# Kernel tuning notes

Measured on AMD Instinct MI355X. Metric: run time of the kernel, lower is better.

## Reference

```python
import jax, jax.numpy as jnp
import numpy as np
import math

B, N, DIM = 2, 4096, 1024
H, D, M = 16, 64, 256


def setup_inputs() -> dict:
    key = jax.random.key(0)
    ks = jax.random.split(key, 6)
    s = 1.0 / math.sqrt(DIM)
    return {
        "x": jax.random.normal(ks[0], (B, N, DIM), dtype=jnp.float32),
        "w_q": jax.random.normal(ks[1], (DIM, H * D), dtype=jnp.float32) * s,
        "w_k": jax.random.normal(ks[2], (DIM, H * D), dtype=jnp.float32) * s,
        "w_v": jax.random.normal(ks[3], (DIM, H * D), dtype=jnp.float32) * s,
        "w_o": jax.random.normal(ks[4], (H * D, DIM), dtype=jnp.float32) * s,
        "b_o": jnp.zeros((DIM,), dtype=jnp.float32),
        "omega": jax.random.normal(ks[5], (M, D), dtype=jnp.float32),
    }


def _heads(t):
    # [B, N, H*D] -> [B, H, N, D]
    return t.reshape(B, N, H, D).transpose(0, 2, 1, 3)


def _phi(t, omega):
    # t: [B,H,N,D], omega: [M,D] -> [B,H,N,M]
    proj = jnp.einsum("bhnd,md->bhnm", t, omega)
    norm = 0.5 * jnp.sum(t * t, axis=-1, keepdims=True)
    return jnp.exp(proj - norm) / math.sqrt(M)


def reference(x, w_q, w_k, w_v, w_o, b_o, omega):
    q = _heads(x @ w_q)
    k = _heads(x @ w_k)
    v = _heads(x @ w_v)
    phi_q = _phi(q, omega)          # [B,H,N,M]
    phi_k = _phi(k, omega)          # [B,H,N,M]
    kv = jnp.einsum("bhnm,bhnd->bhmd", phi_k, v)   # [B,H,M,D]
    k_sum = phi_k.sum(axis=2)                       # [B,H,M]
    z = 1.0 / (jnp.einsum("bhnm,bhm->bhn", phi_q, k_sum) + 1e-6)
    out = jnp.einsum("bhnm,bhmd->bhnd", phi_q, kv) * z[..., None]
    out = out.transpose(0, 2, 1, 3).reshape(B, N, H * D)
    return out @ w_o + b_o
```

## Files before the change

kernel.cpp:

```cpp
#include <hip/hip_runtime.h>

#define DEVI __device__ __forceinline__

using f32x4 = __attribute__((ext_vector_type(4))) float;
using fvec4 = __attribute__((ext_vector_type(4))) float;
using s16x4 = __attribute__((ext_vector_type(4))) short;
using s16x8 = __attribute__((ext_vector_type(8))) short;

DEVI unsigned short f2bf_rn(float f) {
  union { float f; unsigned u; } v; v.f = f;
  unsigned r = v.u + 0x7fffu + ((v.u >> 16) & 1u);
  return (unsigned short)(r >> 16);
}
DEVI float bf2f(unsigned short h) {
  union { unsigned u; float f; } v; v.u = ((unsigned)h) << 16;
  return v.f;
}
DEVI f32x4 mfma16(s16x8 a, s16x8 b, f32x4 c) {
  return __builtin_amdgcn_mfma_f32_16x16x32_bf16(a, b, c, 0, 0, 0);
}

__global__ __launch_bounds__(256) void k_split_x(
    const float* __restrict__ X,
    unsigned short* __restrict__ XH, unsigned short* __restrict__ XL)
{
  size_t i = ((size_t)blockIdx.x * 256 + threadIdx.x) * 8;
  fvec4 a = *(const fvec4*)&X[i];
  fvec4 b = *(const fvec4*)&X[i + 4];
  s16x8 hv, lv;
#pragma unroll
  for (int j = 0; j < 4; ++j) {
    unsigned short h = f2bf_rn(a[j]);
    hv[j] = (short)h; lv[j] = (short)f2bf_rn(a[j] - bf2f(h));
  }
#pragma unroll
  for (int j = 0; j < 4; ++j) {
    unsigned short h = f2bf_rn(b[j]);
    hv[4 + j] = (short)h; lv[4 + j] = (short)f2bf_rn(b[j] - bf2f(h));
  }
  *(s16x8*)&XH[i] = hv;
  *(s16x8*)&XL[i] = lv;
}

__global__ __launch_bounds__(256) void k_prep_w(
    const float* __restrict__ wq, const float* __restrict__ wk,
    const float* __restrict__ wv, const float* __restrict__ wo,
    unsigned short* __restrict__ WTh, unsigned short* __restrict__ WOT)
{
  __shared__ float tile[64][65];
  const int z = blockIdx.z;
  const float* src = (z == 0) ? wq : (z == 1) ? wk : (z == 2) ? wv : wo;
  const int k0 = blockIdx.x * 64;
  const int n0 = blockIdx.y * 64;
  const int t = threadIdx.x;
#pragma unroll
  for (int j = 0; j < 4; ++j) {
    int r = (t >> 4) + 16 * j;
    int c = (t & 15) * 4;
    fvec4 v = *(const fvec4*)&src[(size_t)(k0 + r) * 1024 + n0 + c];
#pragma unroll
    for (int i = 0; i < 4; ++i) tile[r][c + i] = v[i];
  }
  __syncthreads();
#pragma unroll
  for (int j = 0; j < 4; ++j) {
    int n = (t >> 4) + 16 * j;
    int kc = (t & 15) * 4;
    s16x4 hv;
#pragma unroll
    for (int i = 0; i < 4; ++i) hv[i] = (short)f2bf_rn(tile[kc + i][n]);
    if (z < 3) {
      *(s16x4*)&WTh[(size_t)(z * 1024 + n0 + n) * 1024 + k0 + kc] = hv;
    } else {
      *(s16x4*)&WOT[(size_t)(n0 + n) * 1024 + k0 + kc] = hv;
    }
  }
}

__global__ __launch_bounds__(256) void k_gemm_qkv(
    const unsigned short* __restrict__ XH, const unsigned short* __restrict__ XL,
    const unsigned short* __restrict__ WTh,
    unsigned short* __restrict__ QH, unsigned short* __restrict__ QL,
    unsigned short* __restrict__ KH, unsigned short* __restrict__ KL,
    unsigned short* __restrict__ VB)
{
  __shared__ unsigned short AH[128][40], AL[128][40], BH[128][40];
  const int cb = blockIdx.x;
  const int rb = blockIdx.y;
  const int t = threadIdx.x;
  const int w = t >> 6, l = t & 63;
  const bool tp = (cb < 16);
  f32x4 acc[4][4];
#pragma unroll
  for (int a = 0; a < 4; ++a)
#pragma unroll
    for (int b = 0; b < 4; ++b) acc[a][b] = (f32x4)0.f;

  for (int ks = 0; ks < 32; ++ks) {
    const int k0 = ks * 32;
    {
      int r = t >> 1, c = (t & 1) * 16;
      size_t o = (size_t)(rb * 128 + r) * 1024 + k0 + c;
      *(s16x8*)&AH[r][c]     = *(const s16x8*)&XH[o];
      *(s16x8*)&AH[r][c + 8] = *(const s16x8*)&XH[o + 8];
      if (tp) {
        *(s16x8*)&AL[r][c]     = *(const s16x8*)&XL[o];
        *(s16x8*)&AL[r][c + 8] = *(const s16x8*)&XL[o + 8];
      }
      size_t ob = (size_t)(cb * 128 + r) * 1024 + k0 + c;
      *(s16x8*)&BH[r][c]     = *(const s16x8*)&WTh[ob];
      *(s16x8*)&BH[r][c + 8] = *(const s16x8*)&WTh[ob + 8];
    }
    __syncthreads();
    const int wm = (w & 1) * 64, wn = (w >> 1) * 64;
    const int lr = l & 15, ko = (l >> 4) * 8;
    s16x8 ah[4], al[4], bh[4];
#pragma unroll
    for (int f = 0; f < 4; ++f) {
      ah[f] = *(const s16x8*)&AH[wm + f * 16 + lr][ko];
      bh[f] = *(const s16x8*)&BH[wn + f * 16 + lr][ko];
    }
    if (tp) {
#pragma unroll
      for (int f = 0; f < 4; ++f) al[f] = *(const s16x8*)&AL[wm + f * 16 + lr][ko];
    }
#pragma unroll
    for (int fa = 0; fa < 4; ++fa)
#pragma unroll
      for (int fb = 0; fb < 4; ++fb) {
        acc[fa][fb] = mfma16(ah[fa], bh[fb], acc[fa][fb]);
        if (tp) acc[fa][fb] = mfma16(al[fa], bh[fb], acc[fa][fb]);
      }
    __syncthreads();
  }
  const int wm = (w & 1) * 64, wn = (w >> 1) * 64;
  const int lr = l & 15, lg = l >> 4;
#pragma unroll
  for (int fa = 0; fa < 4; ++fa)
#pragma unroll
    for (int r = 0; r < 4; ++r) {
      int row = rb * 128 + wm + fa * 16 + lg * 4 + r;
#pragma unroll
      for (int fb = 0; fb < 4; ++fb) {
        int col = cb * 128 + wn + fb * 16 + lr;
        float v = acc[fa][fb][r];
        unsigned short hs = f2bf_rn(v);
        if (cb < 8) {
          QH[(size_t)row * 1024 + col] = hs;
          QL[(size_t)row * 1024 + col] = f2bf_rn(v - bf2f(hs));
        } else if (cb < 16) {
          KH[(size_t)row * 1024 + col - 1024] = hs;
          KL[(size_t)row * 1024 + col - 1024] = f2bf_rn(v - bf2f(hs));
        } else {
          VB[(size_t)row * 1024 + col - 2048] = hs;
        }
      }
    }
}

__global__ __launch_bounds__(512, 1) void k_phik_kv(
    const unsigned short* __restrict__ KH, const unsigned short* __restrict__ KL,
    const unsigned short* __restrict__ VB,
    const float* __restrict__ omega, float* __restrict__ KVP)
{
  __shared__ unsigned short OH[256][72];
  __shared__ unsigned short KHs[64][72], KLs[64][72];
  __shared__ unsigned short PKT[256][72];
  __shared__ unsigned short AVT[80][72];
  __shared__ float norm_s[64];
  const int nc = blockIdx.x;
  const int bh = blockIdx.y;
  const int b = bh >> 4, h = bh & 15;
  const int t = threadIdx.x, w = t >> 6, l = t & 63;
  const int lr = l & 15, lg = l >> 4, ko8 = lg * 8;

#pragma unroll
  for (int j = 0; j < 8; ++j) {
    int e = j * 512 + t;
    int m = e >> 4, c = (e & 15) * 4;
    fvec4 v = *(const fvec4*)&omega[m * 64 + c];
    s16x4 hv;
#pragma unroll
    for (int i = 0; i < 4; ++i) hv[i] = (short)f2bf_rn(v[i]);
    *(s16x4*)&OH[m][c] = hv;
  }
  for (int e = t; e < 16 * 64; e += 512) {
    int rr = e >> 6, cc = e & 63;
    AVT[64 + rr][cc] = (rr == 0) ? (unsigned short)0x3F80 : (unsigned short)0;
  }

  f32x4 acc2[5][2];
#pragma unroll
  for (int a = 0; a < 5; ++a)
#pragma unroll
    for (int bb = 0; bb < 2; ++bb) acc2[a][bb] = (f32x4)0.f;

  for (int st = 0; st < 8; ++st) {
    const int n0 = nc * 512 + st * 64;
    __syncthreads();
    {
      int r = t >> 3, c8 = (t & 7) * 8;
      size_t o = (size_t)(b * 4096 + n0 + r) * 1024 + h * 64 + c8;
      s16x8 vh = *(const s16x8*)&KH[o];
      s16x8 vl = *(const s16x8*)&KL[o];
      *(s16x8*)&KHs[r][c8] = vh;
      *(s16x8*)&KLs[r][c8] = vl;
      float ss = 0.f;
#pragma unroll
      for (int i = 0; i < 8; ++i) {
        float q = bf2f((unsigned short)vh[i]) + bf2f((unsigned short)vl[i]);
        ss += q * q;
      }
      ss += __shfl_xor(ss, 1);
      ss += __shfl_xor(ss, 2);
      ss += __shfl_xor(ss, 4);
      if ((t & 7) == 0) norm_s[r] = 0.5f * ss;
    }
    {
      int n = t >> 3, dq = (t & 7) * 8;
      s16x8 v = *(const s16x8*)&VB[(size_t)(b * 4096 + n0 + n) * 1024 + h * 64 + dq];
#pragma unroll
      for (int i = 0; i < 8; ++i) AVT[dq + i][n] = (unsigned short)v[i];
    }
    __syncthreads();
    f32x4 acc[4][2];
#pragma unroll
    for (int a = 0; a < 4; ++a)
#pragma unroll
      for (int bb = 0; bb < 2; ++bb) acc[a][bb] = (f32x4)0.f;
#pragma unroll
    for (int ksub = 0; ksub < 2; ++ksub) {
      int ko = ksub * 32 + ko8;
      s16x8 ah[4], al[4], bh[2];
#pragma unroll
      for (int f = 0; f < 4; ++f) {
        ah[f] = *(const s16x8*)&KHs[f * 16 + lr][ko];
        al[f] = *(const s16x8*)&KLs[f * 16 + lr][ko];
      }
#pragma unroll
      for (int f = 0; f < 2; ++f) bh[f] = *(const s16x8*)&OH[w * 32 + f * 16 + lr][ko];
#pragma unroll
      for (int fa = 0; fa < 4; ++fa)
#pragma unroll
        for (int fb = 0; fb < 2; ++fb) {
          acc[fa][fb] = mfma16(ah[fa], bh[fb], acc[fa][fb]);
          acc[fa][fb] = mfma16(al[fa], bh[fb], acc[fa][fb]);
        }
    }
#pragma unroll
    for (int fa = 0; fa < 4; ++fa)
#pragma unroll
      for (int r = 0; r < 4; ++r) {
        int n = fa * 16 + lg * 4 + r;
        float nm = norm_s[n];
#pragma unroll
        for (int fb = 0; fb < 2; ++fb) {
          int m = w * 32 + fb * 16 + lr;
          float p = __expf(acc[fa][fb][r] - nm) * 0.0625f;
          PKT[m][n] = f2bf_rn(p);
        }
      }
    __syncthreads();
#pragma unroll
    for (int ksub = 0; ksub < 2; ++ksub) {
      int ko = ksub * 32 + ko8;
      s16x8 fA[5], fB[2];
#pragma unroll
      for (int f = 0; f < 5; ++f) fA[f] = *(const s16x8*)&AVT[f * 16 + lr][ko];
#pragma unroll
      for (int f = 0; f < 2; ++f) fB[f] = *(const s16x8*)&PKT[w * 32 + f * 16 + lr][ko];
#pragma unroll
      for (int fa = 0; fa < 5; ++fa)
#pragma unroll
        for (int fb = 0; fb < 2; ++fb) acc2[fa][fb] = mfma16(fA[fa], fB[fb], acc2[fa][fb]);
    }
  }
#pragma unroll
  for (int fa = 0; fa < 5; ++fa)
#pragma unroll
    for (int r = 0; r < 4; ++r) {
      int dp = fa * 16 + lg * 4 + r;
#pragma unroll
      for (int fb = 0; fb < 2; ++fb) {
        int m = w * 32 + fb * 16 + lr;
        KVP[(size_t)((bh * 8 + nc) * 80 + dp) * 256 + m] = acc2[fa][fb][r];
      }
    }
}

__global__ __launch_bounds__(256) void k_kv_reduce(
    const float* __restrict__ KVP, float* __restrict__ KVT)
{
  int idx = blockIdx.x * 256 + threadIdx.x;
  if (idx >= 32 * 80 * 256) return;
  int bh = idx / (80 * 256);
  int rem = idx % (80 * 256);
  float s = 0.f;
#pragma unroll
  for (int nci = 0; nci < 8; ++nci) s += KVP[(size_t)(bh * 8 + nci) * 80 * 256 + rem];
  KVT[idx] = s;
}

__global__ __launch_bounds__(256) void k_phi_q(
    const unsigned short* __restrict__ QH, const unsigned short* __restrict__ QL,
    const float* __restrict__ omega,
    unsigned short* __restrict__ PHIQ)
{
  __shared__ unsigned short AHs[64][72], ALs[64][72];
  __shared__ unsigned short OH[256][72];
  __shared__ float norm_s[64];
  const int nt = blockIdx.x;
  const int bh = blockIdx.y;
  const int t = threadIdx.x, w = t >> 6, l = t & 63;
  const int b = bh >> 4, h = bh & 15;
  {
    int r = t >> 2, cq = (t & 3) * 4;
    float ss = 0.f;
#pragma unroll
    for (int j = 0; j < 4; ++j) {
      int c = cq + 16 * j;
      size_t o = (size_t)(b * 4096 + nt * 64 + r) * 1024 + h * 64 + c;
      s16x4 vh = *(const s16x4*)&QH[o];
      s16x4 vl = *(const s16x4*)&QL[o];
      *(s16x4*)&AHs[r][c] = vh;
      *(s16x4*)&ALs[r][c] = vl;
#pragma unroll
      for (int i = 0; i < 4; ++i) {
        float q = bf2f((unsigned short)vh[i]) + bf2f((unsigned short)vl[i]);
        ss += q * q;
      }
    }
    ss += __shfl_xor(ss, 1);
    ss += __shfl_xor(ss, 2);
    if ((t & 3) == 0) norm_s[r] = 0.5f * ss;
  }
#pragma unroll
  for (int j = 0; j < 16; ++j) {
    int e = j * 256 + t;
    int m = e >> 4, c = (e & 15) * 4;
    fvec4 v = *(const fvec4*)&omega[m * 64 + c];
    s16x4 hv;
#pragma unroll
    for (int i = 0; i < 4; ++i) hv[i] = (short)f2bf_rn(v[i]);
    *(s16x4*)&OH[m][c] = hv;
  }
  __syncthreads();
  f32x4 acc[4][4];
#pragma unroll
  for (int a = 0; a < 4; ++a)
#pragma unroll
    for (int bb = 0; bb < 4; ++bb) acc[a][bb] = (f32x4)0.f;
  const int lr = l & 15, ko8 = (l >> 4) * 8;
#pragma unroll
  for (int ksub = 0; ksub < 2; ++ksub) {
    int ko = ksub * 32 + ko8;
    s16x8 ah[4], al[4], bh[4];
#pragma unroll
    for (int f = 0; f < 4; ++f) {
      ah[f] = *(const s16x8*)&AHs[f * 16 + lr][ko];
      al[f] = *(const s16x8*)&ALs[f * 16 + lr][ko];
      bh[f] = *(const s16x8*)&OH[w * 64 + f * 16 + lr][ko];
    }
#pragma unroll
    for (int fa = 0; fa < 4; ++fa)
#pragma unroll
      for (int fb = 0; fb < 4; ++fb) {
        acc[fa][fb] = mfma16(ah[fa], bh[fb], acc[fa][fb]);
        acc[fa][fb] = mfma16(al[fa], bh[fb], acc[fa][fb]);
      }
  }
  const int lg = l >> 4;
#pragma unroll
  for (int fa = 0; fa < 4; ++fa)
#pragma unroll
    for (int r = 0; r < 4; ++r) {
      int n = fa * 16 + lg * 4 + r;
      float nm = norm_s[n];
#pragma unroll
      for (int fb = 0; fb < 4; ++fb) {
        int m = w * 64 + fb * 16 + lr;
        float p = __expf(acc[fa][fb][r] - nm) * 0.0625f;
        PHIQ[(size_t)(bh * 4096 + nt * 64 + n) * 256 + m] = f2bf_rn(p);
      }
    }
}

__global__ __launch_bounds__(256) void k_attn(
    const unsigned short* __restrict__ PHIQ,
    const float* __restrict__ KVT,
    unsigned short* __restrict__ ATT)
{
  __shared__ unsigned short KVB[80][264];
  __shared__ unsigned short PH[128][40];
  const int ntile = blockIdx.x;
  const int bh = blockIdx.y;
  const int b = bh >> 4, h = bh & 15;
  const int t = threadIdx.x, w = t >> 6, l = t & 63;
#pragma unroll
  for (int j = 0; j < 20; ++j) {
    int e = (j * 256 + t) * 4;
    int dp = e >> 8, m = e & 255;
    fvec4 v = *(const fvec4*)&KVT[(size_t)bh * 80 * 256 + dp * 256 + m];
    s16x4 hv;
#pragma unroll
    for (int i = 0; i < 4; ++i) hv[i] = (short)f2bf_rn(v[i]);
    *(s16x4*)&KVB[dp][m] = hv;
  }
  __syncthreads();
  f32x4 acc[2][5];
#pragma unroll
  for (int a = 0; a < 2; ++a)
#pragma unroll
    for (int bb = 0; bb < 5; ++bb) acc[a][bb] = (f32x4)0.f;
  for (int ks = 0; ks < 8; ++ks) {
    const int m0 = ks * 32;
#pragma unroll
    for (int j = 0; j < 2; ++j) {
      int n = t >> 1, c = (t & 1) * 8 + j * 16;
      *(s16x8*)&PH[n][c] =
          *(const s16x8*)&PHIQ[(size_t)(bh * 4096 + ntile * 128 + n) * 256 + m0 + c];
    }
    __syncthreads();
    const int lr = l & 15, ko = (l >> 4) * 8;
    s16x8 fA[2], fB[5];
#pragma unroll
    for (int f = 0; f < 2; ++f) fA[f] = *(const s16x8*)&PH[w * 32 + f * 16 + lr][ko];
#pragma unroll
    for (int f = 0; f < 5; ++f) fB[f] = *(const s16x8*)&KVB[f * 16 + lr][m0 + ko];
#pragma unroll
    for (int fa = 0; fa < 2; ++fa)
#pragma unroll
      for (int fb = 0; fb < 5; ++fb) acc[fa][fb] = mfma16(fA[fa], fB[fb], acc[fa][fb]);
    __syncthreads();
  }
  const int lr = l & 15, lg = l >> 4;
#pragma unroll
  for (int fa = 0; fa < 2; ++fa)
#pragma unroll
    for (int r = 0; r < 4; ++r) {
      float den = __shfl(acc[fa][4][r], (l & 48));
      float z = 1.f / (den + 1e-6f);
      int n = ntile * 128 + w * 32 + fa * 16 + lg * 4 + r;
#pragma unroll
      for (int fb = 0; fb < 4; ++fb) {
        int col = h * 64 + fb * 16 + lr;
        ATT[(size_t)(b * 4096 + n) * 1024 + col] = f2bf_rn(acc[fa][fb][r] * z);
      }
    }
}

__global__ __launch_bounds__(256) void k_gemm_out(
    const unsigned short* __restrict__ ATT,
    const unsigned short* __restrict__ WOT,
    const float* __restrict__ b_o,
    float* __restrict__ OUT)
{
  __shared__ unsigned short As[128][40], Bs[128][40];
  const int cb = blockIdx.x;
  const int rb = blockIdx.y;
  const int t = threadIdx.x, w = t >> 6, l = t & 63;
  f32x4 acc[4][4];
#pragma unroll
  for (int a = 0; a < 4; ++a)
#pragma unroll
    for (int bb = 0; bb < 4; ++bb) acc[a][bb] = (f32x4)0.f;
  for (int ks = 0; ks < 32; ++ks) {
    const int k0 = ks * 32;
#pragma unroll
    for (int j = 0; j < 2; ++j) {
      int r = t >> 1, c = (t & 1) * 8 + j * 16;
      *(s16x8*)&As[r][c] = *(const s16x8*)&ATT[(size_t)(rb * 128 + r) * 1024 + k0 + c];
      *(s16x8*)&Bs[r][c] = *(const s16x8*)&WOT[(size_t)(cb * 128 + r) * 1024 + k0 + c];
    }
    __syncthreads();
    const int wm = (w & 1) * 64, wn = (w >> 1) * 64, lr = l & 15, ko = (l >> 4) * 8;
    s16x8 fA[4], fB[4];
#pragma unroll
    for (int f = 0; f < 4; ++f) {
      fA[f] = *(const s16x8*)&As[wm + f * 16 + lr][ko];
      fB[f] = *(const s16x8*)&Bs[wn + f * 16 + lr][ko];
    }
#pragma unroll
    for (int fa = 0; fa < 4; ++fa)
#pragma unroll
      for (int fb = 0; fb < 4; ++fb) acc[fa][fb] = mfma16(fA[fa], fB[fb], acc[fa][fb]);
    __syncthreads();
  }
  const int wm = (w & 1) * 64, wn = (w >> 1) * 64, lr = l & 15, lg = l >> 4;
#pragma unroll
  for (int fa = 0; fa < 4; ++fa)
#pragma unroll
    for (int r = 0; r < 4; ++r) {
      int row = rb * 128 + wm + fa * 16 + lg * 4 + r;
#pragma unroll
      for (int fb = 0; fb < 4; ++fb) {
        int col = cb * 128 + wn + fb * 16 + lr;
        OUT[(size_t)row * 1024 + col] = acc[fa][fb][r] + b_o[col];
      }
    }
}

extern "C" void kernel_launch(void* const* d_in, const int* in_sizes, int n_in,
                              void* d_out, int out_size, void* d_ws, size_t ws_size,
                              hipStream_t stream)
{
  const float* x  = (const float*)d_in[0];
  const float* wq = (const float*)d_in[1];
  const float* wk = (const float*)d_in[2];
  const float* wv = (const float*)d_in[3];
  const float* wo = (const float*)d_in[4];
  const float* bo = (const float*)d_in[5];
  const float* om = (const float*)d_in[6];
  float* out = (float*)d_out;

  const size_t PLANE = (size_t)8192 * 1024 * 2;
  char* ws = (char*)d_ws;
  unsigned short* WOT = (unsigned short*)(ws);
  char* segB = ws + 2097152;
  char* segC = segB + 2 * PLANE;
  char* segD = segC + 4 * PLANE;
  char* segE = segD + 26214400;

  unsigned short* QH  = (unsigned short*)segB;
  unsigned short* QL  = (unsigned short*)(segB + PLANE);
  unsigned short* ATT = (unsigned short*)segB;

  unsigned short* KH  = (unsigned short*)segC;
  unsigned short* KL  = (unsigned short*)(segC + PLANE);
  unsigned short* VB  = (unsigned short*)(segC + 2 * PLANE);
  unsigned short* XH  = (unsigned short*)(segC + 3 * PLANE);
  unsigned short* PHIQ = (unsigned short*)segC;

  unsigned short* WTh = (unsigned short*)segD;
  unsigned short* XL  = (unsigned short*)(segD + 6291456);
  float* KVP = (float*)segD;
  float* KVT = (float*)segE;

  k_split_x<<<dim3(4096), 256, 0, stream>>>(x, XH, XL);
  k_prep_w<<<dim3(16, 16, 4), 256, 0, stream>>>(wq, wk, wv, wo, WTh, WOT);
  k_gemm_qkv<<<dim3(24, 64), 256, 0, stream>>>(XH, XL, WTh, QH, QL, KH, KL, VB);
  k_phik_kv<<<dim3(8, 32), 512, 0, stream>>>(KH, KL, VB, om, KVP);
  k_kv_reduce<<<dim3(2560), 256, 0, stream>>>(KVP, KVT);
  k_phi_q<<<dim3(64, 32), 256, 0, stream>>>(QH, QL, om, PHIQ);
  k_attn<<<dim3(32, 32), 256, 0, stream>>>(PHIQ, KVT, ATT);
  k_gemm_out<<<dim3(8, 64), 256, 0, stream>>>(ATT, WOT, bo, out);
}
```

Baseline: 256.3 us.

## Fuse phi_q with attention and use direct global-to-LDS loads in GEMMs

Merges the phi(Q) feature-map kernel and the attention kernel, so phi_q stays in shared memory instead of going through a global buffer. QKV and output GEMMs now stage tiles with global_load_lds 16-byte loads into unpadded LDS. This removes the PHIQ global round trip and register staging. In exchange, the fused kernel uses a large LDS footprint, which limits occupancy, and the unpadded layout may cause bank conflicts.

```diff
diff --git a/kernel.cpp b/kernel.cpp
--- a/kernel.cpp
+++ b/kernel.cpp
@@ -18,6 +18,11 @@
 }
 DEVI f32x4 mfma16(s16x8 a, s16x8 b, f32x4 c) {
   return __builtin_amdgcn_mfma_f32_16x16x32_bf16(a, b, c, 0, 0, 0);
+}
+DEVI void gld16(const void* g, void* lds) {
+  __builtin_amdgcn_global_load_lds(
+      (const __attribute__((address_space(1))) unsigned int*)g,
+      (__attribute__((address_space(3))) unsigned int*)lds, 16, 0, 0);
 }
 
 __global__ __launch_bounds__(256) void k_split_x(
@@ -84,7 +89,7 @@
     unsigned short* __restrict__ KH, unsigned short* __restrict__ KL,
     unsigned short* __restrict__ VB)
 {
-  __shared__ unsigned short AH[128][40], AL[128][40], BH[128][40];
+  __shared__ unsigned short AH[128 * 32], AL[128 * 32], BH[128 * 32];
   const int cb = blockIdx.x;
   const int rb = blockIdx.y;
   const int t = threadIdx.x;
@@ -96,33 +101,43 @@
 #pragma unroll
     for (int b = 0; b < 4; ++b) acc[a][b] = (f32x4)0.f;
 
+  const int r0 = w * 32;
+  const int lrow = l >> 2;
+  const int lcol = (l & 3) * 8;
+  const size_t gA0 = (size_t)(rb * 128 + r0 + lrow) * 1024 + lcol;
+  const size_t gA1 = gA0 + (size_t)16 * 1024;
+  const size_t gB0 = (size_t)(cb * 128 + r0 + lrow) * 1024 + lcol;
+  const size_t gB1 = gB0 + (size_t)16 * 1024;
+  unsigned short* ldsA0 = &AH[r0 * 32];
+  unsigned short* ldsA1 = &AH[(r0 + 16) * 32];
+  unsigned short* ldsL0 = &AL[r0 * 32];
+  unsigned short* ldsL1 = &AL[(r0 + 16) * 32];
+  unsigned short* ldsB0 = &BH[r0 * 32];
+  unsigned short* ldsB1 = &BH[(r0 + 16) * 32];
+
+  const int wm = (w & 1) * 64, wn = (w >> 1) * 64;
+  const int lr = l & 15, ko = (l >> 4) * 8;
+
   for (int ks = 0; ks < 32; ++ks) {
     const int k0 = ks * 32;
-    {
-      int r = t >> 1, c = (t & 1) * 16;
-      size_t o = (size_t)(rb * 128 + r) * 1024 + k0 + c;
-      *(s16x8*)&AH[r][c]     = *(const s16x8*)&XH[o];
-      *(s16x8*)&AH[r][c + 8] = *(const s16x8*)&XH[o + 8];
-      if (tp) {
-        *(s16x8*)&AL[r][c]     = *(const s16x8*)&XL[o];
-        *(s16x8*)&AL[r][c + 8] = *(const s16x8*)&XL[o + 8];
-      }
-      size_t ob = (size_t)(cb * 128 + r) * 1024 + k0 + c;
-      *(s16x8*)&BH[r][c]     = *(const s16x8*)&WTh[ob];
-      *(s16x8*)&BH[r][c + 8] = *(const s16x8*)&WTh[ob + 8];
-    }
-    __syncthreads();
-    const int wm = (w & 1) * 64, wn = (w >> 1) * 64;
-    const int lr = l & 15, ko = (l >> 4) * 8;
+    gld16(&XH[gA0 + k0], ldsA0);
+    gld16(&XH[gA1 + k0], ldsA1);
+    if (tp) {
+      gld16(&XL[gA0 + k0], ldsL0);
+      gld16(&XL[gA1 + k0], ldsL1);
+    }
+    gld16(&WTh[gB0 + k0], ldsB0);
+    gld16(&WTh[gB1 + k0], ldsB1);
+    __syncthreads();
     s16x8 ah[4], al[4], bh[4];
 #pragma unroll
     for (int f = 0; f < 4; ++f) {
-      ah[f] = *(const s16x8*)&AH[wm + f * 16 + lr][ko];
-      bh[f] = *(const s16x8*)&BH[wn + f * 16 + lr][ko];
+      ah[f] = *(const s16x8*)&AH[(wm + f * 16 + lr) * 32 + ko];
+      bh[f] = *(const s16x8*)&BH[(wn + f * 16 + lr) * 32 + ko];
     }
     if (tp) {
 #pragma unroll
-      for (int f = 0; f < 4; ++f) al[f] = *(const s16x8*)&AL[wm + f * 16 + lr][ko];
+      for (int f = 0; f < 4; ++f) al[f] = *(const s16x8*)&AL[(wm + f * 16 + lr) * 32 + ko];
     }
 #pragma unroll
     for (int fa = 0; fa < 4; ++fa)
@@ -133,8 +148,7 @@
       }
     __syncthreads();
   }
-  const int wm = (w & 1) * 64, wn = (w >> 1) * 64;
-  const int lr = l & 15, lg = l >> 4;
+  const int lg = l >> 4;
 #pragma unroll
   for (int fa = 0; fa < 4; ++fa)
 #pragma unroll
@@ -301,18 +315,22 @@
   KVT[idx] = s;
 }
 
-__global__ __launch_bounds__(256) void k_phi_q(
-    const unsigned short* __restrict__ QH, const unsigned short* __restrict__ QL,
-    const float* __restrict__ omega,
-    unsigned short* __restrict__ PHIQ)
-{
-  __shared__ unsigned short AHs[64][72], ALs[64][72];
+__global__ __launch_bounds__(256) void k_phiq_attn(
+    const unsigned short* QH, const unsigned short* QL,
+    const float* __restrict__ omega, const float* __restrict__ KVT,
+    unsigned short* ATT)
+{
+  __shared__ unsigned short QHs[64][72], QLs[64][72];
   __shared__ unsigned short OH[256][72];
+  __shared__ unsigned short PQ[64][264];
+  __shared__ unsigned short KVB[80][264];
   __shared__ float norm_s[64];
   const int nt = blockIdx.x;
   const int bh = blockIdx.y;
   const int t = threadIdx.x, w = t >> 6, l = t & 63;
   const int b = bh >> 4, h = bh & 15;
+  const int lr = l & 15, lg = l >> 4, ko8 = lg * 8;
+
   {
     int r = t >> 2, cq = (t & 3) * 4;
     float ss = 0.f;
@@ -322,8 +340,8 @@
       size_t o = (size_t)(b * 4096 + nt * 64 + r) * 1024 + h * 64 + c;
       s16x4 vh = *(const s16x4*)&QH[o];
       s16x4 vl = *(const s16x4*)&QL[o];
-      *(s16x4*)&AHs[r][c] = vh;
-      *(s16x4*)&ALs[r][c] = vl;
+      *(s16x4*)&QHs[r][c] = vh;
+      *(s16x4*)&QLs[r][c] = vl;
 #pragma unroll
       for (int i = 0; i < 4; ++i) {
         float q = bf2f((unsigned short)vh[i]) + bf2f((unsigned short)vl[i]);
@@ -344,58 +362,6 @@
     for (int i = 0; i < 4; ++i) hv[i] = (short)f2bf_rn(v[i]);
     *(s16x4*)&OH[m][c] = hv;
   }
-  __syncthreads();
-  f32x4 acc[4][4];
-#pragma unroll
-  for (int a = 0; a < 4; ++a)
-#pragma unroll
-    for (int bb = 0; bb < 4; ++bb) acc[a][bb] = (f32x4)0.f;
-  const int lr = l & 15, ko8 = (l >> 4) * 8;
-#pragma unroll
-  for (int ksub = 0; ksub < 2; ++ksub) {
-    int ko = ksub * 32 + ko8;
-    s16x8 ah[4], al[4], bh[4];
-#pragma unroll
-    for (int f = 0; f < 4; ++f) {
-      ah[f] = *(const s16x8*)&AHs[f * 16 + lr][ko];
-      al[f] = *(const s16x8*)&ALs[f * 16 + lr][ko];
-      bh[f] = *(const s16x8*)&OH[w * 64 + f * 16 + lr][ko];
-    }
-#pragma unroll
-    for (int fa = 0; fa < 4; ++fa)
-#pragma unroll
-      for (int fb = 0; fb < 4; ++fb) {
-        acc[fa][fb] = mfma16(ah[fa], bh[fb], acc[fa][fb]);
-        acc[fa][fb] = mfma16(al[fa], bh[fb], acc[fa][fb]);
-      }
-  }
-  const int lg = l >> 4;
-#pragma unroll
-  for (int fa = 0; fa < 4; ++fa)
-#pragma unroll
-    for (int r = 0; r < 4; ++r) {
-      int n = fa * 16 + lg * 4 + r;
-      float nm = norm_s[n];
-#pragma unroll
-      for (int fb = 0; fb < 4; ++fb) {
-        int m = w * 64 + fb * 16 + lr;
-        float p = __expf(acc[fa][fb][r] - nm) * 0.0625f;
-        PHIQ[(size_t)(bh * 4096 + nt * 64 + n) * 256 + m] = f2bf_rn(p);
-      }
-    }
-}
-
-__global__ __launch_bounds__(256) void k_attn(
-    const unsigned short* __restrict__ PHIQ,
-    const float* __restrict__ KVT,
-    unsigned short* __restrict__ ATT)
-{
-  __shared__ unsigned short KVB[80][264];
-  __shared__ unsigned short PH[128][40];
-  const int ntile = blockIdx.x;
-  const int bh = blockIdx.y;
-  const int b = bh >> 4, h = bh & 15;
-  const int t = threadIdx.x, w = t >> 6, l = t & 63;
 #pragma unroll
   for (int j = 0; j < 20; ++j) {
     int e = (j * 256 + t) * 4;
@@ -407,46 +373,66 @@
     *(s16x4*)&KVB[dp][m] = hv;
   }
   __syncthreads();
-  f32x4 acc[2][5];
-#pragma unroll
-  for (int a = 0; a < 2; ++a)
-#pragma unroll
-    for (int bb = 0; bb < 5; ++bb) acc[a][bb] = (f32x4)0.f;
+  f32x4 acc[4][4];
+#pragma unroll
+  for (int a = 0; a < 4; ++a)
+#pragma unroll
+    for (int bb = 0; bb < 4; ++bb) acc[a][bb] = (f32x4)0.f;
+#pragma unroll
+  for (int ksub = 0; ksub < 2; ++ksub) {
+    int ko = ksub * 32 + ko8;
+    s16x8 ah[4], al[4], bh[4];
+#pragma unroll
+    for (int f = 0; f < 4; ++f) {
+      ah[f] = *(const s16x8*)&QHs[f * 16 + lr][ko];
+      al[f] = *(const s16x8*)&QLs[f * 16 + lr][ko];
+      bh[f] = *(const s16x8*)&OH[w * 64 + f * 16 + lr][ko];
+    }
+#pragma unroll
+    for (int fa = 0; fa < 4; ++fa)
+#pragma unroll
+      for (int fb = 0; fb < 4; ++fb) {
+        acc[fa][fb] = mfma16(ah[fa], bh[fb], acc[fa][fb]);
+        acc[fa][fb] = mfma16(al[fa], bh[fb], acc[fa][fb]);
+      }
+  }
+#pragma unroll
+  for (int fa = 0; fa < 4; ++fa)
+#pragma unroll
+    for (int r = 0; r < 4; ++r) {
+      int n = fa * 16 + lg * 4 + r;
+      float nm = norm_s[n];
+#pragma unroll
+      for (int fb = 0; fb < 4; ++fb) {
+        int m = w * 64 + fb * 16 + lr;
+        float p = __expf(acc[fa][fb][r] - nm) * 0.0625f;
+        PQ[n][m] = f2bf_rn(p);
+      }
+    }
+  __syncthreads();
+  f32x4 acc2[5];
+#pragma unroll
+  for (int bb = 0; bb < 5; ++bb) acc2[bb] = (f32x4)0.f;
   for (int ks = 0; ks < 8; ++ks) {
     const int m0 = ks * 32;
-#pragma unroll
-    for (int j = 0; j < 2; ++j) {
-      int n = t >> 1, c = (t & 1) * 8 + j * 16;
-      *(s16x8*)&PH[n][c] =
-          *(const s16x8*)&PHIQ[(size_t)(bh * 4096 + ntile * 128 + n) * 256 + m0 + c];
-    }
-    __syncthreads();
-    const int lr = l & 15, ko = (l >> 4) * 8;
-    s16x8 fA[2], fB[5];
-#pragma unroll
-    for (int f = 0; f < 2; ++f) fA[f] = *(const s16x8*)&PH[w * 32 + f * 16 + lr][ko];
-#pragma unroll
-    for (int f = 0; f < 5; ++f) fB[f] = *(const s16x8*)&KVB[f * 16 + lr][m0 + ko];
-#pragma unroll
-    for (int fa = 0; fa < 2; ++fa)
-#pragma unroll
-      for (int fb = 0; fb < 5; ++fb) acc[fa][fb] = mfma16(fA[fa], fB[fb], acc[fa][fb]);
-    __syncthreads();
-  }
-  const int lr = l & 15, lg = l >> 4;
-#pragma unroll
-  for (int fa = 0; fa < 2; ++fa)
-#pragma unroll
-    for (int r = 0; r < 4; ++r) {
-      float den = __shfl(acc[fa][4][r], (l & 48));
-      float z = 1.f / (den + 1e-6f);
-      int n = ntile * 128 + w * 32 + fa * 16 + lg * 4 + r;
-#pragma unroll
-      for (int fb = 0; fb < 4; ++fb) {
-        int col = h * 64 + fb * 16 + lr;
-        ATT[(size_t)(b * 4096 + n) * 1024 + col] = f2bf_rn(acc[fa][fb][r] * z);
-      }
-    }
+    s16x8 fA = *(const s16x8*)&PQ[w * 16 + lr][m0 + ko8];
+    s16x8 fB[5];
+#pragma unroll
+    for (int f = 0; f < 5; ++f) fB[f] = *(const s16x8*)&KVB[f * 16 + lr][m0 + ko8];
+#pragma unroll
+    for (int fb = 0; fb < 5; ++fb) acc2[fb] = mfma16(fA, fB[fb], acc2[fb]);
+  }
+#pragma unroll
+  for (int r = 0; r < 4; ++r) {
+    float den = __shfl(acc2[4][r], (l & 48));
+    float z = 1.f / (den + 1e-6f);
+    int n = nt * 64 + w * 16 + lg * 4 + r;
+#pragma unroll
+    for (int fb = 0; fb < 4; ++fb) {
+      int col = h * 64 + fb * 16 + lr;
+      ATT[(size_t)(b * 4096 + n) * 1024 + col] = f2bf_rn(acc2[fb][r] * z);
+    }
+  }
 }
 
 __global__ __launch_bounds__(256) void k_gemm_out(
@@ -455,7 +441,7 @@
     const float* __restrict__ b_o,
     float* __restrict__ OUT)
 {
-  __shared__ unsigned short As[128][40], Bs[128][40];
+  __shared__ unsigned short As[128 * 32], Bs[128 * 32];
   const int cb = blockIdx.x;
   const int rb = blockIdx.y;
   const int t = threadIdx.x, w = t >> 6, l = t & 63;
@@ -464,21 +450,34 @@
   for (int a = 0; a < 4; ++a)
 #pragma unroll
     for (int bb = 0; bb < 4; ++bb) acc[a][bb] = (f32x4)0.f;
+
+  const int r0 = w * 32;
+  const int lrow = l >> 2;
+  const int lcol = (l & 3) * 8;
+  const size_t gA0 = (size_t)(rb * 128 + r0 + lrow) * 1024 + lcol;
+  const size_t gA1 = gA0 + (size_t)16 * 1024;
+  const size_t gB0 = (size_t)(cb * 128 + r0 + lrow) * 1024 + lcol;
+  const size_t gB1 = gB0 + (size_t)16 * 1024;
+  unsigned short* ldsA0 = &As[r0 * 32];
+  unsigned short* ldsA1 = &As[(r0 + 16) * 32];
+  unsigned short* ldsB0 = &Bs[r0 * 32];
+  unsigned short* ldsB1 = &Bs[(r0 + 16) * 32];
+
+  const int wm = (w & 1) * 64, wn = (w >> 1) * 64;
+  const int lr = l & 15, ko = (l >> 4) * 8;
+
   for (int ks = 0; ks < 32; ++ks) {
     const int k0 = ks * 32;
-#pragma unroll
-    for (int j = 0; j < 2; ++j) {
-      int r = t >> 1, c = (t & 1) * 8 + j * 16;
-      *(s16x8*)&As[r][c] = *(const s16x8*)&ATT[(size_t)(rb * 128 + r) * 1024 + k0 + c];
-      *(s16x8*)&Bs[r][c] = *(const s16x8*)&WOT[(size_t)(cb * 128 + r) * 1024 + k0 + c];
-    }
-    __syncthreads();
-    const int wm = (w & 1) * 64, wn = (w >> 1) * 64, lr = l & 15, ko = (l >> 4) * 8;
+    gld16(&ATT[gA0 + k0], ldsA0);
+    gld16(&ATT[gA1 + k0], ldsA1);
+    gld16(&WOT[gB0 + k0], ldsB0);
+    gld16(&WOT[gB1 + k0], ldsB1);
+    __syncthreads();
     s16x8 fA[4], fB[4];
 #pragma unroll
     for (int f = 0; f < 4; ++f) {
-      fA[f] = *(const s16x8*)&As[wm + f * 16 + lr][ko];
-      fB[f] = *(const s16x8*)&Bs[wn + f * 16 + lr][ko];
+      fA[f] = *(const s16x8*)&As[(wm + f * 16 + lr) * 32 + ko];
+      fB[f] = *(const s16x8*)&Bs[(wn + f * 16 + lr) * 32 + ko];
     }
 #pragma unroll
     for (int fa = 0; fa < 4; ++fa)
@@ -486,7 +485,7 @@
       for (int fb = 0; fb < 4; ++fb) acc[fa][fb] = mfma16(fA[fa], fB[fb], acc[fa][fb]);
     __syncthreads();
   }
-  const int wm = (w & 1) * 64, wn = (w >> 1) * 64, lr = l & 15, lg = l >> 4;
+  const int lg = l >> 4;
 #pragma unroll
   for (int fa = 0; fa < 4; ++fa)
 #pragma unroll
@@ -529,7 +528,6 @@
   unsigned short* KL  = (unsigned short*)(segC + PLANE);
   unsigned short* VB  = (unsigned short*)(segC + 2 * PLANE);
   unsigned short* XH  = (unsigned short*)(segC + 3 * PLANE);
-  unsigned short* PHIQ = (unsigned short*)segC;
 
   unsigned short* WTh = (unsigned short*)segD;
   unsigned short* XL  = (unsigned short*)(segD + 6291456);
@@ -541,7 +539,6 @@
   k_gemm_qkv<<<dim3(24, 64), 256, 0, stream>>>(XH, XL, WTh, QH, QL, KH, KL, VB);
   k_phik_kv<<<dim3(8, 32), 512, 0, stream>>>(KH, KL, VB, om, KVP);
   k_kv_reduce<<<dim3(2560), 256, 0, stream>>>(KVP, KVT);
-  k_phi_q<<<dim3(64, 32), 256, 0, stream>>>(QH, QL, om, PHIQ);
-  k_attn<<<dim3(32, 32), 256, 0, stream>>>(PHIQ, KVT, ATT);
+  k_phiq_attn<<<dim3(64, 32), 256, 0, stream>>>(QH, QL, om, KVT, ATT);
   k_gemm_out<<<dim3(8, 64), 256, 0, stream>>>(ATT, WOT, bo, out);
 }
```

Result: faster. 233.3 us (-9.0%).
